# Kernel tuning notes

Measured on AMD Instinct MI355X. Metric: run time of the kernel, lower is better.

Reference implementation:

```python
import jax, jax.numpy as jnp
import numpy as np
import math

H_HEADS = 4
SQRT_2_PI = math.sqrt(2.0 / math.pi)


def _gelu_tanh(x):
    return 0.5 * x * (1.0 + jnp.tanh(SQRT_2_PI * (x + 0.044715 * x ** 3)))


def _ln(x, g, b, eps=1e-5):
    mu = jnp.mean(x, axis=-1, keepdims=True)
    var = jnp.var(x, axis=-1, keepdims=True)
    return g * (x - mu) * jax.lax.rsqrt(var + eps) + b


def _forward(support_emb_mat, query_t, support_t, cls_embed, t_freq, t_phase,
             Wq, bq, Wk, bk, Wv, bv, Wo, bo, ln1_g, ln1_b, time_w,
             W1, b1, W2, b2, ln2_g, ln2_b, Wc, bc, bn_g, bn_b):
    B, F, MD = support_emb_mat.shape
    Q = query_t.shape[1]
    S = F + 1
    H = H_HEADS
    D = MD * H
    dph = D // H
    L = Wq.shape[0]
    BQ = B * Q

    # [CLS] + support sequence, feature-tiled to model_dim*num_heads
    cls = jnp.broadcast_to(cls_embed, (B, 1, MD))
    seq = jnp.concatenate([cls, support_emb_mat], axis=1)          # [B,S,MD]
    x = jnp.tile(seq, (1, 1, H))                                    # [B,S,D]
    x = jnp.broadcast_to(x[:, None], (B, Q, S, D)).reshape(BQ, S, D)

    # time sequence: [query_t_q, support_t...] per (b,q)
    sup = jnp.broadcast_to(support_t[:, None, :], (B, Q, F))
    t_seq = jnp.concatenate([query_t[..., None], sup], axis=-1).reshape(BQ, S)
    t_diff = t_seq[:, :, None] - t_seq[:, None, :]                  # [BQ,S,S]
    # time encoder: cos(t*freq + phase) -> [BQ,S,S,TD]
    t_emb = jnp.cos(t_diff[..., None] * t_freq + t_phase)

    # scale as in source: (dim_per_head // num_heads) ** -0.5
    scale = (dph // H) ** (-0.5)

    for l in range(L):
        bias = t_emb @ time_w[l]                                    # [BQ,S,S]
        add = jnp.tile(bias, (H, 1, 1))                             # [BQ*H,S,S]
        res = x
        # raw row-major reshape to (BQ*H, S, dph) exactly as torch .view
        q = (x @ Wq[l] + bq[l]).reshape(BQ * H, S, dph)
        k = (x @ Wk[l] + bk[l]).reshape(BQ * H, S, dph)
        v = (x @ Wv[l] + bv[l]).reshape(BQ * H, S, dph)
        attn = jax.nn.softmax(jnp.einsum('bsd,btd->bst', q, k) * scale + add, axis=-1)
        ctx = jnp.einsum('bst,btd->bsd', attn, v).reshape(BQ, S, D)
        out = _ln(res + ctx @ Wo[l] + bo[l], ln1_g[l], ln1_b[l])
        ffn = _gelu_tanh(out @ W1[l] + b1[l]) @ W2[l] + b2[l]
        x = _ln(out + ffn, ln2_g[l], ln2_b[l])

    # compress: Linear -> BatchNorm1d over seq channels (train mode) -> LeakyReLU
    h = x @ Wc + bc                                                 # [BQ,S,MD]
    mu = jnp.mean(h, axis=(0, 2), keepdims=True)
    var = jnp.var(h, axis=(0, 2), keepdims=True)
    h = bn_g[None, :, None] * (h - mu) * jax.lax.rsqrt(var + 1e-5) + bn_b[None, :, None]
    h = jnp.where(h >= 0, h, 0.01 * h)                              # LeakyReLU
    return h[:, 0, :].reshape(B, Q, MD)


def setup_inputs() -> dict:
    key = jax.random.key(0)
    ks = jax.random.split(key, 24)
    B, Q, F, MD = 128, 32, 7, 128
    H, L, FFN, TD = 4, 6, 2048, 32
    S = F + 1
    D = MD * H

    def nrm(k, shape, s=0.02):
        return jax.random.normal(k, shape, jnp.float32) * s

    inp = {
        'support_emb_mat': jax.random.normal(ks[0], (B, F, MD), jnp.float32),
        'query_t': jax.random.uniform(ks[1], (B, Q), jnp.float32) * 100.0,
        'support_t': jax.random.uniform(ks[2], (B, F), jnp.float32) * 100.0,
        'cls_embed': jax.random.uniform(ks[3], (1, MD), jnp.float32),
        't_freq': nrm(ks[4], (TD,), 1.0),
        't_phase': nrm(ks[5], (TD,), 1.0),
        'Wq': nrm(ks[6], (L, D, D)), 'bq': jnp.zeros((L, D)),
        'Wk': nrm(ks[7], (L, D, D)), 'bk': jnp.zeros((L, D)),
        'Wv': nrm(ks[8], (L, D, D)), 'bv': jnp.zeros((L, D)),
        'Wo': nrm(ks[9], (L, D, D)), 'bo': jnp.zeros((L, D)),
        'ln1_g': jnp.ones((L, D)), 'ln1_b': jnp.zeros((L, D)),
        'time_w': jnp.ones((L, TD)) * 0.001,
        'W1': nrm(ks[10], (L, D, FFN)), 'b1': jnp.zeros((L, FFN)),
        'W2': nrm(ks[11], (L, FFN, D)), 'b2': jnp.zeros((L, D)),
        'ln2_g': jnp.ones((L, D)), 'ln2_b': jnp.zeros((L, D)),
        'Wc': nrm(ks[12], (D, MD)), 'bc': jnp.zeros((MD,)),
        'bn_g': jnp.ones((S,)), 'bn_b': jnp.zeros((S,)),
    }
    return inp


def reference(support_emb_mat, query_t, support_t, cls_embed, t_freq, t_phase,
              Wq, bq, Wk, bk, Wv, bv, Wo, bo, ln1_g, ln1_b, time_w,
              W1, b1, W2, b2, ln2_g, ln2_b, Wc, bc, bn_g, bn_b):
    return _forward(support_emb_mat, query_t, support_t, cls_embed, t_freq, t_phase,
                    Wq, bq, Wk, bk, Wv, bv, Wo, bo, ln1_g, ln1_b, time_w,
                    W1, b1, W2, b2, ln2_g, ln2_b, Wc, bc, bn_g, bn_b)
```

## Files before the change

### kernel.cpp

```cpp
#include <hip/hip_runtime.h>
#include <hip/hip_bf16.h>

typedef _Float16 f16;
typedef __attribute__((ext_vector_type(8))) _Float16 f16x8;
typedef __attribute__((ext_vector_type(4))) _Float16 f16x4;
typedef __attribute__((ext_vector_type(4))) float f32x4;

#define DEVI __device__ __forceinline__

DEVI float ldf(const void* p, size_t i, int isf32) {
    if (isf32) return ((const float*)p)[i];
    unsigned int u = ((const unsigned short*)p)[i];
    union { unsigned int b; float f; } c; c.b = u << 16;
    return c.f;
}

DEVI void gld_lds16(const f16* g, f16* l) {
    __builtin_amdgcn_global_load_lds(
        (__attribute__((address_space(1))) void*)(g),
        (__attribute__((address_space(3))) void*)(l), 16, 0, 0);
}

__global__ void detect_dtype(const void* qt, int* flag) {
    if (threadIdx.x == 0 && blockIdx.x == 0) {
        const unsigned int* w = (const unsigned int*)qt;
        int cnt = 0;
        for (int i = 0; i < 64; ++i) {
            unsigned int lo = w[i] & 0xFFFFu;
            union { unsigned int b; float f; } c; c.b = lo << 16;
            if (c.f >= 1e-4f && c.f <= 100.5f) ++cnt;
        }
        *flag = (cnt >= 32) ? 0 : 1;
    }
}

__global__ __launch_bounds__(256)
void cvt_in(const void* __restrict__ src, float* __restrict__ dst, int n,
            const int* __restrict__ flag) {
    const int f32 = *flag;
    int i = blockIdx.x * 256 + threadIdx.x;
    if (i < n) dst[i] = ldf(src, i, f32);
}

__global__ __launch_bounds__(256)
void fill_out(float* out, float v) {
    out[blockIdx.x * 256 + threadIdx.x] = v;
}

template<int EPI>
__global__ __launch_bounds__(512, 2)
void gemm256(const f16* __restrict__ Ag, const f16* __restrict__ BTg,
             const float* __restrict__ biasg, void* __restrict__ outg,
             int NZ, int gridN, int N, int K, int lda,
             long zsB, long zsBias, long zsC)
{
    const int tid = threadIdx.x;
    const int w = tid >> 6, lane = tid & 63;
    const int wm = w >> 2, wn = w & 3;
    const int r16 = lane & 15, q4 = lane >> 4;

    const int cpx = gridDim.x >> 3;
    const int id  = (blockIdx.x & 7) * cpx + (blockIdx.x >> 3);

    const int nz   = id % NZ;
    const int mloc = id / NZ;
    const int z    = nz / gridN;
    const int nt   = nz - z * gridN;
    const int tm = mloc * 256, tn = nt * 256;

    const f16*   BT   = BTg + (size_t)z * zsB;
    const float* bias = biasg + (size_t)z * zsBias;
    const size_t zoffC = (size_t)z * zsC;

    __shared__ __align__(16) f16 smA[2][2][16][64][8];
    __shared__ __align__(16) f16 smB[2][2][16][64][8];

    const f16* gA[4]; const f16* gB[4];
#pragma unroll
    for (int t = 0; t < 4; ++t) {
        const int c = 4 * w + t, kk = c >> 4, rc = c & 15;
        gA[t] = Ag + (size_t)(tm + rc * 16 + r16) * lda + kk * 32 + q4 * 8;
        gB[t] = BT + (size_t)(tn + rc * 16 + r16) * K  + kk * 32 + q4 * 8;
    }
    f16* const smAbase = &smA[0][0][0][0][0];
    f16* const smBbase = &smB[0][0][0][0][0];
    const int coff = (4 * w) * 512;

    auto issue = [&](int kt, int buf) {
        const size_t o = (size_t)kt * 64;
        const int bo = buf * 16384 + coff;
#pragma unroll
        for (int t = 0; t < 4; ++t) {
            gld_lds16(gA[t] + o, smAbase + bo + t * 512);
            gld_lds16(gB[t] + o, smBbase + bo + t * 512);
        }
    };

    f32x4 acc[8][4];
#pragma unroll
    for (int i = 0; i < 8; ++i)
#pragma unroll
        for (int j = 0; j < 4; ++j) acc[i][j] = (f32x4)0.0f;

    const int iters = K >> 6;
    issue(0, 0);
    __builtin_amdgcn_s_waitcnt(0x0F70);
    __builtin_amdgcn_s_barrier();
    __asm__ __volatile__("" ::: "memory");

    for (int kt = 0; kt < iters; ++kt) {
        const int cur = kt & 1;
        const bool more = (kt + 1 < iters);
        if (more) issue(kt + 1, cur ^ 1);
#pragma unroll
        for (int kk = 0; kk < 2; ++kk) {
            f16x8 af[8], bf[4];
#pragma unroll
            for (int i = 0; i < 8; ++i)
                af[i] = *(const f16x8*)&smA[cur][kk][wm * 8 + i][lane][0];
#pragma unroll
            for (int j = 0; j < 4; ++j)
                bf[j] = *(const f16x8*)&smB[cur][kk][wn * 4 + j][lane][0];
#pragma unroll
            for (int i = 0; i < 8; ++i)
#pragma unroll
                for (int j = 0; j < 4; ++j)
                    acc[i][j] = __builtin_amdgcn_mfma_f32_16x16x32_f16(
                        bf[j], af[i], acc[i][j], 0, 0, 0);
        }
        if (more) {
            __builtin_amdgcn_s_waitcnt(0x0F70);
            __builtin_amdgcn_s_barrier();
            __asm__ __volatile__("" ::: "memory");
        }
    }

    const int rowBase = tm + wm * 128;
    const int colBase = tn + wn * 64;
#pragma unroll
    for (int i = 0; i < 8; ++i) {
        const int row = rowBase + i * 16 + r16;
        const size_t rowoff = (size_t)row * N;
#pragma unroll
        for (int j = 0; j < 4; ++j) {
            const int n0 = colBase + j * 16 + q4 * 4;
            const f32x4 bv4 = *(const f32x4*)&bias[n0];
            f16x4 o;
#pragma unroll
            for (int r = 0; r < 4; ++r) {
                float v = acc[i][j][r] + bv4[r];
                if constexpr (EPI == 2) {
                    float v2 = v * v;
                    float t  = v * (1.0f + 0.044715f * v2);
                    float e  = __expf(1.5957691216057308f * t);
                    float rc = __builtin_amdgcn_rcpf(e + 1.0f);
                    v = v - v * rc;
                }
                o[r] = (f16)v;
            }
            *(f16x4*)((f16*)outg + zoffC + rowoff + n0) = o;
        }
    }
}

template<int EPI>
__global__ __launch_bounds__(256, 4)
void gemm_bt(const f16* __restrict__ Ag, const f16* __restrict__ BTg,
             const float* __restrict__ biasg, const f16* __restrict__ resg,
             void* __restrict__ outg,
             int NT, int NTZ, int MCHUNK, int MT, int N, int K, int lda,
             long zsB, long zsBias, long zsC)
{
    const int tid  = threadIdx.x;
    const int w    = tid >> 6, lane = tid & 63;
    const int wm   = w >> 1,   wn   = w & 1;

    const int id    = blockIdx.x;
    const int pc    = MCHUNK * NTZ;
    const int chunk = id / pc;
    const int rem   = id - chunk * pc;
    const int mloc  = rem % MCHUNK;
    const int ynz   = rem / MCHUNK;
    const int z     = ynz / NT;
    const int tmB   = (chunk * MCHUNK + mloc) * (128 * MT);
    const int tn    = (ynz - z * NT) * 128;

    const f16*   BT   = BTg + (size_t)z * zsB;
    const float* bias = biasg + (size_t)z * zsBias;
    const size_t zoffC = (size_t)z * zsC;

    __shared__ __align__(16) f16 smA[2][8][64][8];
    __shared__ __align__(16) f16 smB[2][8][64][8];

    const int r16 = lane & 15, q4 = lane >> 4;
    const int iters = K >> 5;

    const f16* gA0 = Ag + (size_t)(tmB + (2 * w) * 16 + r16) * lda + q4 * 8;
    const f16* gA1 = gA0 + (size_t)16 * lda;
    const f16* gB0 = BT + (size_t)(tn + (2 * w) * 16 + r16) * K + q4 * 8;
    const f16* gB1 = gB0 + (size_t)16 * K;

    auto issue = [&](int msN, int ktN, int buf) {
        const size_t aoff = (size_t)msN * 128 * lda + (size_t)ktN * 32;
        const size_t boff = (size_t)ktN * 32;
        gld_lds16(gA0 + aoff, &smA[buf][2 * w][0][0]);
        gld_lds16(gA1 + aoff, &smA[buf][2 * w + 1][0][0]);
        gld_lds16(gB0 + boff, &smB[buf][2 * w][0][0]);
        gld_lds16(gB1 + boff, &smB[buf][2 * w + 1][0][0]);
    };

    issue(0, 0, 0);
    int stage = 0;

    for (int ms = 0; ms < MT; ++ms) {
        const int tm = tmB + ms * 128;

        f32x4 acc[4][4];
#pragma unroll
        for (int i = 0; i < 4; ++i)
#pragma unroll
            for (int j = 0; j < 4; ++j) acc[i][j] = (f32x4)0.0f;

        for (int kt = 0; kt < iters; ++kt, ++stage) {
            const int cur = stage & 1;
            __builtin_amdgcn_s_barrier();
            int ktN = kt + 1, msN = ms;
            if (ktN == iters) { ktN = 0; ++msN; }
            if (msN < MT) {
                issue(msN, ktN, cur ^ 1);
                __builtin_amdgcn_s_waitcnt(0x0F74);
            } else {
                __builtin_amdgcn_s_waitcnt(0x0F70);
            }
            __builtin_amdgcn_s_barrier();
            __asm__ __volatile__("" ::: "memory");

            f16x8 af[4], bf[4];
#pragma unroll
            for (int i = 0; i < 4; ++i) {
                af[i] = *(const f16x8*)&smA[cur][wm * 4 + i][lane][0];
                bf[i] = *(const f16x8*)&smB[cur][wn * 4 + i][lane][0];
            }
#pragma unroll
            for (int i = 0; i < 4; ++i)
#pragma unroll
                for (int j = 0; j < 4; ++j)
                    acc[i][j] = __builtin_amdgcn_mfma_f32_16x16x32_f16(
                        bf[j], af[i], acc[i][j], 0, 0, 0);
        }

        const int rowBase = tm + wm * 64;
        const int colBase = tn + wn * 64;
#pragma unroll
        for (int i = 0; i < 4; ++i) {
            const int row = rowBase + i * 16 + r16;
            const size_t rowoff = (size_t)row * N;
#pragma unroll
            for (int j = 0; j < 4; ++j) {
                const int n0 = colBase + j * 16 + q4 * 4;
                const f32x4 bv4 = *(const f32x4*)&bias[n0];
                if constexpr (EPI == 3) {
                    f32x4 o;
#pragma unroll
                    for (int r = 0; r < 4; ++r) o[r] = acc[i][j][r] + bv4[r];
                    *(f32x4*)((float*)outg + rowoff + n0) = o;
                } else {
                    f16x4 o;
#pragma unroll
                    for (int r = 0; r < 4; ++r) {
                        float v = acc[i][j][r] + bv4[r];
                        if constexpr (EPI == 2) {
                            float v2 = v * v;
                            float t  = v * (1.0f + 0.044715f * v2);
                            float e  = __expf(1.5957691216057308f * t);
                            float rc = __builtin_amdgcn_rcpf(e + 1.0f);
                            v = v - v * rc;
                        }
                        o[r] = (f16)v;
                    }
                    *(f16x4*)((f16*)outg + zoffC + rowoff + n0) = o;
                }
            }
        }
    }
}

__global__ __launch_bounds__(512, 2)
void gemm_ln(const f16* __restrict__ Ag, const f16* __restrict__ BTg,
             const float* __restrict__ bias, const f16* __restrict__ resg,
             const float* __restrict__ lng, const float* __restrict__ lnb,
             f16* __restrict__ Yg, int K, int lda)
{
    const int tid = threadIdx.x;
    const int w = tid >> 6, lane = tid & 63;
    const int wm = w >> 2, wn = w & 3;
    const int r16 = lane & 15, q4 = lane >> 4;
    const int tm = blockIdx.x * 128;

    __shared__ __align__(16) f16 smA[2][8][64][8];
    __shared__ __align__(16) f16 smB[2][32][64][8];
    __shared__ __align__(16) float lnS[128][4];
    __shared__ __align__(16) float lnQ[128][4];

    f32x4 acc[4][8];
#pragma unroll
    for (int i = 0; i < 4; ++i)
#pragma unroll
        for (int j = 0; j < 8; ++j) acc[i][j] = (f32x4)0.0f;

    const f16* gA  = Ag  + (size_t)(tm + w * 16 + r16) * lda + q4 * 8;
    const f16* gB  = BTg + (size_t)(w * 64 + r16) * K + q4 * 8;
    const int iters = K >> 5;

    auto issue = [&](int kt, int buf) {
        const size_t o = (size_t)kt * 32;
        gld_lds16(gA + o, &smA[buf][w][0][0]);
#pragma unroll
        for (int t = 0; t < 4; ++t)
            gld_lds16(gB + (size_t)(t * 16) * K + o, &smB[buf][w * 4 + t][0][0]);
    };

    issue(0, 0);
    for (int kt = 0; kt < iters; ++kt) {
        const int cur = kt & 1;
        __builtin_amdgcn_s_barrier();
        if (kt + 1 < iters) {
            issue(kt + 1, cur ^ 1);
            __builtin_amdgcn_s_waitcnt(0x0F75);
        } else {
            __builtin_amdgcn_s_waitcnt(0x0F70);
        }
        __builtin_amdgcn_s_barrier();
        __asm__ __volatile__("" ::: "memory");

        f16x8 af[4], bf[8];
#pragma unroll
        for (int i = 0; i < 4; ++i)
            af[i] = *(const f16x8*)&smA[cur][wm * 4 + i][lane][0];
#pragma unroll
        for (int j = 0; j < 8; ++j)
            bf[j] = *(const f16x8*)&smB[cur][wn * 8 + j][lane][0];
#pragma unroll
        for (int i = 0; i < 4; ++i)
#pragma unroll
            for (int j = 0; j < 8; ++j)
                acc[i][j] = __builtin_amdgcn_mfma_f32_16x16x32_f16(
                    bf[j], af[i], acc[i][j], 0, 0, 0);
    }

    const int rowB = wm * 64;
    const int colB = wn * 128;

    float ps[4], pq[4];
#pragma unroll
    for (int i = 0; i < 4; ++i) {
        const int grow = tm + rowB + i * 16 + r16;
        const size_t roff = (size_t)grow * 512;
        float s = 0.f, sq = 0.f;
#pragma unroll
        for (int j = 0; j < 8; ++j) {
            const int n0 = colB + j * 16 + q4 * 4;
            const f32x4 biv = *(const f32x4*)&bias[n0];
            const f16x4 rv  = *(const f16x4*)&resg[roff + n0];
#pragma unroll
            for (int r = 0; r < 4; ++r) {
                float v = acc[i][j][r] + biv[r] + (float)rv[r];
                acc[i][j][r] = v;
                s += v; sq += v * v;
            }
        }
        s  += __shfl_xor(s, 16, 64);  s  += __shfl_xor(s, 32, 64);
        sq += __shfl_xor(sq, 16, 64); sq += __shfl_xor(sq, 32, 64);
        ps[i] = s; pq[i] = sq;
    }
    if (q4 == 0) {
#pragma unroll
        for (int i = 0; i < 4; ++i) {
            const int lr = rowB + i * 16 + r16;
            lnS[lr][wn] = ps[i];
            lnQ[lr][wn] = pq[i];
        }
    }
    __syncthreads();

#pragma unroll
    for (int i = 0; i < 4; ++i) {
        const int lr = rowB + i * 16 + r16;
        const f32x4 s4 = *(const f32x4*)&lnS[lr][0];
        const f32x4 q4v = *(const f32x4*)&lnQ[lr][0];
        const float s  = s4[0] + s4[1] + s4[2] + s4[3];
        const float sq = q4v[0] + q4v[1] + q4v[2] + q4v[3];
        const float mu = s * (1.0f / 512.0f);
        const float var = sq * (1.0f / 512.0f) - mu * mu;
        const float rs = rsqrtf(var + 1e-5f);
        const size_t rowoff = (size_t)(tm + lr) * 512;
#pragma unroll
        for (int j = 0; j < 8; ++j) {
            const int n0 = colB + j * 16 + q4 * 4;
            const f32x4 g4 = *(const f32x4*)&lng[n0];
            const f32x4 b4 = *(const f32x4*)&lnb[n0];
            f16x4 o;
#pragma unroll
            for (int r = 0; r < 4; ++r)
                o[r] = (f16)(g4[r] * (acc[i][j][r] - mu) * rs + b4[r]);
            *(f16x4*)&Yg[rowoff + n0] = o;
        }
    }
}

__global__ __launch_bounds__(256)
void attn_kernel(const f16* __restrict__ qg, const f16* __restrict__ kg,
                 const f16* __restrict__ vg, const float* __restrict__ biasL,
                 f16* __restrict__ cg, int small)
{
    const int w = threadIdx.x >> 6, lane = threadIdx.x & 63;
    const int j = blockIdx.x * 4 + w;
    __shared__ __align__(16) f16 sQ[4][8][136];
    __shared__ __align__(16) f16 sK[4][8][136];
    __shared__ __align__(16) f16 sV[4][8][136];
    __shared__ float sP[4][8][8];

    const size_t base  = (size_t)j * 1024;
    const size_t ibase = small ? ((size_t)(j >> 7) * 4096 + (size_t)(j & 3) * 1024)
                               : base;
#pragma unroll
    for (int t = 0; t < 2; ++t) {
        int flat = (t * 64 + lane) * 8;
        int r = flat >> 7, c = flat & 127;
        *(f16x8*)&sQ[w][r][c] = *(const f16x8*)(qg + ibase + flat);
        *(f16x8*)&sK[w][r][c] = *(const f16x8*)(kg + ibase + flat);
        *(f16x8*)&sV[w][r][c] = *(const f16x8*)(vg + ibase + flat);
    }
    __syncthreads();

    const int i = lane >> 3, jj = lane & 7;
    float d = 0.f;
#pragma unroll
    for (int c = 0; c < 16; ++c) {
        f16x8 qv = *(const f16x8*)&sQ[w][i][c * 8];
        f16x8 kv = *(const f16x8*)&sK[w][jj][c * 8];
#pragma unroll
        for (int e = 0; e < 8; ++e) d += (float)qv[e] * (float)kv[e];
    }
    float s = d * 0.17677669529663687f + biasL[(size_t)(j & 4095) * 64 + lane];
    float mx = s;
    mx = fmaxf(mx, __shfl_xor(mx, 1, 64));
    mx = fmaxf(mx, __shfl_xor(mx, 2, 64));
    mx = fmaxf(mx, __shfl_xor(mx, 4, 64));
    float p = __expf(s - mx);
    float sum = p;
    sum += __shfl_xor(sum, 1, 64);
    sum += __shfl_xor(sum, 2, 64);
    sum += __shfl_xor(sum, 4, 64);
    sP[w][i][jj] = p / sum;
    __syncthreads();

#pragma unroll
    for (int t2 = 0; t2 < 8; ++t2) {
        float ap[8];
#pragma unroll
        for (int e = 0; e < 8; ++e) ap[e] = sP[w][t2][e];
#pragma unroll
        for (int h = 0; h < 2; ++h) {
            int flat = (t2 * 2 + h) * 64 + lane;
            int dd = flat & 127;
            float o = 0.f;
#pragma unroll
            for (int e = 0; e < 8; ++e) o += ap[e] * (float)sV[w][e][dd];
            cg[base + flat] = (f16)o;
        }
    }
}

__global__ __launch_bounds__(256)
void build_x0(const void* __restrict__ sup, const void* __restrict__ cls,
              f16* __restrict__ xb, const int* __restrict__ flag)
{
    const int f32 = *flag;
    const size_t idx = ((size_t)blockIdx.x * 256 + threadIdx.x) * 4;
    const int row = (int)(idx >> 9), col0 = (int)(idx & 511);
    const int s = row & 7, b = row >> 8;
    f16x4 o;
#pragma unroll
    for (int e = 0; e < 4; ++e) {
        const int md = (col0 + e) & 127;
        float v = (s == 0) ? ldf(cls, md, f32)
                           : ldf(sup, ((size_t)b * 7 + (s - 1)) * 128 + md, f32);
        o[e] = (f16)v;
    }
    *(f16x4*)(xb + idx) = o;
}

__global__ __launch_bounds__(256)
void build_x0s(const void* __restrict__ sup, const void* __restrict__ cls,
               f16* __restrict__ xs, const int* __restrict__ flag)
{
    const int f32 = *flag;
    const size_t idx = ((size_t)blockIdx.x * 256 + threadIdx.x) * 4;
    const int row = (int)(idx >> 9), col0 = (int)(idx & 511);
    const int s = row & 7, b = row >> 3;
    f16x4 o;
#pragma unroll
    for (int e = 0; e < 4; ++e) {
        const int md = (col0 + e) & 127;
        float v = (s == 0) ? ldf(cls, md, f32)
                           : ldf(sup, ((size_t)b * 7 + (s - 1)) * 128 + md, f32);
        o[e] = (f16)v;
    }
    *(f16x4*)(xs + idx) = o;
}

__global__ __launch_bounds__(256)
void bias_kernel(const void* __restrict__ qt, const void* __restrict__ st,
                 const void* __restrict__ freq, const void* __restrict__ phase,
                 const void* __restrict__ tw, float* __restrict__ biasAll,
                 const int* __restrict__ flag)
{
    const int f32 = *flag;
    const int lane = threadIdx.x & 63;
    const int bq = blockIdx.x * 4 + (threadIdx.x >> 6);
    const int b = bq >> 5, qq = bq & 31;
    const int i = lane >> 3, jj = lane & 7;
    const float ti = (i  == 0) ? ldf(qt, b * 32 + qq, f32) : ldf(st, b * 7 + i  - 1, f32);
    const float tj = (jj == 0) ? ldf(qt, b * 32 + qq, f32) : ldf(st, b * 7 + jj - 1, f32);
    const float td = ti - tj;
    float a[6] = {0.f, 0.f, 0.f, 0.f, 0.f, 0.f};
    for (int t = 0; t < 32; ++t) {
        float c = __cosf(td * ldf(freq, t, f32) + ldf(phase, t, f32));
#pragma unroll
        for (int l = 0; l < 6; ++l) a[l] += c * ldf(tw, l * 32 + t, f32);
    }
#pragma unroll
    for (int l = 0; l < 6; ++l)
        biasAll[(size_t)l * (4096 * 64) + (size_t)bq * 64 + lane] = a[l];
}

__global__ __launch_bounds__(256)
void transpose_cvt(const void* __restrict__ W, f16* __restrict__ WT,
                   int K, int N, long zsW, long zsWT, const int* __restrict__ flag)
{
    const int f32 = *flag;
    const size_t zoff = (size_t)blockIdx.z * zsW;
    f16* WTz = WT + (size_t)blockIdx.z * zsWT;
    __shared__ float tile[64][65];
    const int tn = blockIdx.x * 64, tk = blockIdx.y * 64;
#pragma unroll
    for (int t = 0; t < 16; ++t) {
        int idx = t * 256 + threadIdx.x;
        int r = idx >> 6, c = idx & 63;
        tile[r][c] = ldf(W, zoff + (size_t)(tk + r) * N + tn + c, f32);
    }
    __syncthreads();
#pragma unroll
    for (int t = 0; t < 16; ++t) {
        int idx = t * 256 + threadIdx.x;
        int r = idx >> 6, c = idx & 63;
        WTz[(size_t)(tn + r) * K + tk + c] = (f16)tile[c][r];
    }
}

__global__ __launch_bounds__(256)
void gather_qkvb(const void* __restrict__ bq, const void* __restrict__ bk,
                 const void* __restrict__ bv, float* __restrict__ dst,
                 const int* __restrict__ flag)
{
    const int f32 = *flag;
    int i = blockIdx.x * 256 + threadIdx.x;
    if (i < 9216) {
        int z = i / 3072, rem = i % 3072;
        const void* src = (z == 0) ? bq : ((z == 1) ? bk : bv);
        dst[i] = ldf(src, rem, f32);
    }
}

__global__ __launch_bounds__(256)
void bn_reduce(const float* __restrict__ h0, float* __restrict__ stats)
{
    const int t = blockIdx.x * 256 + threadIdx.x;
    float s = 0.f, ss = 0.f;
#pragma unroll
    for (int k = 0; k < 8; ++k) {
        float v = h0[t + k * 65536];
        s += v; ss += v * v;
    }
#pragma unroll
    for (int m = 1; m <= 32; m <<= 1) {
        s  += __shfl_xor(s, m, 64);
        ss += __shfl_xor(ss, m, 64);
    }
    __shared__ float ls[8];
    const int w = threadIdx.x >> 6, lane = threadIdx.x & 63;
    if (lane == 0) { ls[w] = s; ls[4 + w] = ss; }
    __syncthreads();
    if (threadIdx.x == 0) {
        atomicAdd(&stats[0], ls[0] + ls[1] + ls[2] + ls[3]);
        atomicAdd(&stats[1], ls[4] + ls[5] + ls[6] + ls[7]);
    }
}

__global__ __launch_bounds__(256)
void bn_apply(const float* __restrict__ h0, const float* __restrict__ stats,
              const float* __restrict__ bnp, float* __restrict__ out)
{
    const int t = blockIdx.x * 256 + threadIdx.x;
    const float mu  = stats[0] * (1.0f / 524288.0f);
    const float var = stats[1] * (1.0f / 524288.0f) - mu * mu;
    const float rs  = rsqrtf(var + 1e-5f);
    float v = bnp[0] * (h0[t] - mu) * rs + bnp[8];
    v = (v >= 0.f) ? v : 0.01f * v;
    out[t] = v;
}

extern "C" void kernel_launch(void* const* d_in, const int* in_sizes, int n_in,
                              void* d_out, int out_size, void* d_ws, size_t ws_size,
                              hipStream_t stream)
{
    (void)in_sizes; (void)n_in; (void)out_size;
    const void* sup   = d_in[0];
    const void* qt    = d_in[1];
    const void* st    = d_in[2];
    const void* cls   = d_in[3];
    const void* freq  = d_in[4];
    const void* phase = d_in[5];
    const void* Wq = d_in[6];  const void* bqv = d_in[7];
    const void* Wk = d_in[8];  const void* bkv = d_in[9];
    const void* Wv = d_in[10]; const void* bvv = d_in[11];
    const void* Wo = d_in[12]; const void* bo  = d_in[13];
    const void* ln1g = d_in[14]; const void* ln1b = d_in[15];
    const void* tw = d_in[16];
    const void* W1 = d_in[17]; const void* b1 = d_in[18];
    const void* W2 = d_in[19]; const void* b2 = d_in[20];
    const void* ln2g = d_in[21]; const void* ln2b = d_in[22];
    const void* Wc = d_in[23]; const void* bc = d_in[24];
    const void* bng = d_in[25]; const void* bnb = d_in[26];

    const size_t NEEDED = 245658240;
    if (ws_size < NEEDED) {
        fill_out<<<2048, 256, 0, stream>>>((float*)d_out, 999.0f);
        return;
    }

    char* ws = (char*)d_ws;
    f16*   wt      = (f16*)(ws + 0);
    float* biasAll = (float*)(ws + 37879808);
    float* qkvb    = (float*)(ws + 44171264);
    float* prm     = (float*)(ws + 44208128);
    float* stats   = (float*)(ws + 44331584);
    int*   flag    = (int*)  (ws + 44331592);
    f16*   xb      = (f16*)(ws + 44331648);
    f16*   ob      = (f16*)(ws + 77886080);
    char*  region  = ws + 111440512;
    f16*   qb      = (f16*)(region);
    f16*   kb      = (f16*)(region + 33554432);
    f16*   vb      = (f16*)(region + 67108864);
    f16*   cb      = (f16*)(region + 100663296);
    f16*   qs      = (f16*)(region);
    f16*   xs      = (f16*)(region + 100663296);
    f16*   fbuf    = (f16*)(region);
    float* h0      = (float*)(region);

    detect_dtype<<<1, 64, 0, stream>>>(qt, flag);

    cvt_in<<<12, 256, 0, stream>>>(bo,   prm + 0,     3072,  flag);
    cvt_in<<<48, 256, 0, stream>>>(b1,   prm + 3072,  12288, flag);
    cvt_in<<<12, 256, 0, stream>>>(b2,   prm + 15360, 3072,  flag);
    cvt_in<<<1,  256, 0, stream>>>(bc,   prm + 18432, 128,   flag);
    cvt_in<<<12, 256, 0, stream>>>(ln1g, prm + 18560, 3072,  flag);
    cvt_in<<<12, 256, 0, stream>>>(ln1b, prm + 21632, 3072,  flag);
    cvt_in<<<12, 256, 0, stream>>>(ln2g, prm + 24704, 3072,  flag);
    cvt_in<<<12, 256, 0, stream>>>(ln2b, prm + 27776, 3072,  flag);
    cvt_in<<<1,  256, 0, stream>>>(bng,  prm + 30848, 8,     flag);
    cvt_in<<<1,  256, 0, stream>>>(bnb,  prm + 30856, 8,     flag);

    transpose_cvt<<<dim3(8, 8, 6),  256, 0, stream>>>(Wq, wt + 0,        512, 512,  262144, 262144, flag);
    transpose_cvt<<<dim3(8, 8, 6),  256, 0, stream>>>(Wk, wt + 1572864,  512, 512,  262144, 262144, flag);
    transpose_cvt<<<dim3(8, 8, 6),  256, 0, stream>>>(Wv, wt + 3145728,  512, 512,  262144, 262144, flag);
    transpose_cvt<<<dim3(8, 8, 6),  256, 0, stream>>>(Wo, wt + 4718592,  512, 512,  262144, 262144, flag);
    transpose_cvt<<<dim3(32, 8, 6), 256, 0, stream>>>(W1, wt + 6291456,  512, 2048, 1048576, 1048576, flag);
    transpose_cvt<<<dim3(8, 32, 6), 256, 0, stream>>>(W2, wt + 12582912, 2048, 512, 1048576, 1048576, flag);
    transpose_cvt<<<dim3(2, 8, 1),  256, 0, stream>>>(Wc, wt + 18874368, 512, 128,  0, 0, flag);
    gather_qkvb<<<36, 256, 0, stream>>>(bqv, bkv, bvv, qkvb, flag);
    build_x0<<<16384, 256, 0, stream>>>(sup, cls, xb, flag);
    build_x0s<<<512, 256, 0, stream>>>(sup, cls, xs, flag);
    bias_kernel<<<1024, 256, 0, stream>>>(qt, st, freq, phase, tw, biasAll, flag);
    hipMemsetAsync(stats, 0, 8, stream);

    for (int l = 0; l < 6; ++l) {
        if (l == 0) {
            gemm256<0><<<24, 512, 0, stream>>>(
                xs, wt, qkvb, qs,
                6, 2, 512, 512, 512, 1572864, 3072, 524288);
            attn_kernel<<<4096, 256, 0, stream>>>(
                qs, qs + 524288, qs + 1048576, biasAll, cb, 1);
        } else {
            gemm256<0><<<768, 512, 0, stream>>>(
                xb, wt + l * 262144, qkvb + l * 512, qb,
                6, 2, 512, 512, 512, 1572864, 3072, 16777216);
            attn_kernel<<<4096, 256, 0, stream>>>(
                qb, kb, vb, biasAll + (size_t)l * 262144, cb, 0);
        }
        gemm_ln<<<256, 512, 0, stream>>>(
            cb, wt + 4718592 + l * 262144, prm + 0 + l * 512, xb,
            prm + 18560 + l * 512, prm + 21632 + l * 512, ob, 512, 512);
        gemm256<2><<<1024, 512, 0, stream>>>(
            ob, wt + 6291456 + l * 1048576, prm + 3072 + l * 2048, fbuf,
            8, 8, 2048, 512, 512, 0, 0, 0);
        gemm_ln<<<256, 512, 0, stream>>>(
            fbuf, wt + 12582912 + l * 1048576, prm + 15360 + l * 512, ob,
            prm + 24704 + l * 512, prm + 27776 + l * 512, xb, 2048, 2048);
    }

    gemm_bt<3><<<32, 256, 0, stream>>>(
        xb, wt + 18874368, prm + 18432, nullptr, h0,
        1, 1, 32, 1, 128, 512, 4096 , 0, 0, 0);
    bn_reduce<<<256, 256, 0, stream>>>(h0, stats);
    bn_apply<<<2048, 256, 0, stream>>>(h0, stats, prm + 30848, (float*)d_out);
}
```

Baseline: 2.837 ms.

## Replace double-buffered K=64 GEMM loop with 4-stage K=32 LDS pipeline

Changes the GEMM mainloop from two LDS buffers holding 64-wide K tiles to four buffers holding 32-wide K tiles, keeping three tiles in flight. Partial vmcnt waits replace the full drain before each barrier, so global-to-LDS loads overlap MFMA work over more stages. The cost is a barrier every 32 K-elements instead of every 64, and fewer MFMAs per barrier. Total LDS size stays the same.

```diff
diff --git a/kernel.cpp b/kernel.cpp
--- a/kernel.cpp
+++ b/kernel.cpp
@@ -72,27 +72,24 @@
     const float* bias = biasg + (size_t)z * zsBias;
     const size_t zoffC = (size_t)z * zsC;
 
-    __shared__ __align__(16) f16 smA[2][2][16][64][8];
-    __shared__ __align__(16) f16 smB[2][2][16][64][8];
-
-    const f16* gA[4]; const f16* gB[4];
-#pragma unroll
-    for (int t = 0; t < 4; ++t) {
-        const int c = 4 * w + t, kk = c >> 4, rc = c & 15;
-        gA[t] = Ag + (size_t)(tm + rc * 16 + r16) * lda + kk * 32 + q4 * 8;
-        gB[t] = BT + (size_t)(tn + rc * 16 + r16) * K  + kk * 32 + q4 * 8;
-    }
-    f16* const smAbase = &smA[0][0][0][0][0];
-    f16* const smBbase = &smB[0][0][0][0][0];
-    const int coff = (4 * w) * 512;
-
-    auto issue = [&](int kt, int buf) {
-        const size_t o = (size_t)kt * 64;
-        const int bo = buf * 16384 + coff;
-#pragma unroll
-        for (int t = 0; t < 4; ++t) {
-            gld_lds16(gA[t] + o, smAbase + bo + t * 512);
-            gld_lds16(gB[t] + o, smBbase + bo + t * 512);
+    __shared__ __align__(16) f16 smA[4][16][64][8];
+    __shared__ __align__(16) f16 smB[4][16][64][8];
+
+    const f16* gA[2]; const f16* gB[2];
+#pragma unroll
+    for (int t = 0; t < 2; ++t) {
+        const int rc = 2 * w + t;
+        gA[t] = Ag + (size_t)(tm + rc * 16 + r16) * lda + q4 * 8;
+        gB[t] = BT + (size_t)(tn + rc * 16 + r16) * K  + q4 * 8;
+    }
+
+    auto issue = [&](int kt) {
+        const int buf = kt & 3;
+        const size_t o = (size_t)kt * 32;
+#pragma unroll
+        for (int t = 0; t < 2; ++t) {
+            gld_lds16(gA[t] + o, &smA[buf][2 * w + t][0][0]);
+            gld_lds16(gB[t] + o, &smB[buf][2 * w + t][0][0]);
         }
     };
 
@@ -102,37 +99,32 @@
 #pragma unroll
         for (int j = 0; j < 4; ++j) acc[i][j] = (f32x4)0.0f;
 
-    const int iters = K >> 6;
-    issue(0, 0);
-    __builtin_amdgcn_s_waitcnt(0x0F70);
-    __builtin_amdgcn_s_barrier();
-    __asm__ __volatile__("" ::: "memory");
+    const int iters = K >> 5;
+    issue(0); issue(1); issue(2);
 
     for (int kt = 0; kt < iters; ++kt) {
-        const int cur = kt & 1;
-        const bool more = (kt + 1 < iters);
-        if (more) issue(kt + 1, cur ^ 1);
-#pragma unroll
-        for (int kk = 0; kk < 2; ++kk) {
-            f16x8 af[8], bf[4];
-#pragma unroll
-            for (int i = 0; i < 8; ++i)
-                af[i] = *(const f16x8*)&smA[cur][kk][wm * 8 + i][lane][0];
+        if (kt + 2 < iters)      __builtin_amdgcn_s_waitcnt(0x0F78);
+        else if (kt + 1 < iters) __builtin_amdgcn_s_waitcnt(0x0F74);
+        else                     __builtin_amdgcn_s_waitcnt(0x0F70);
+        __asm__ __volatile__("" ::: "memory");
+        __builtin_amdgcn_s_barrier();
+        __asm__ __volatile__("" ::: "memory");
+        if (kt + 3 < iters) issue(kt + 3);
+
+        const int cur = kt & 3;
+        f16x8 af[8], bf[4];
+#pragma unroll
+        for (int i = 0; i < 8; ++i)
+            af[i] = *(const f16x8*)&smA[cur][wm * 8 + i][lane][0];
+#pragma unroll
+        for (int j = 0; j < 4; ++j)
+            bf[j] = *(const f16x8*)&smB[cur][wn * 4 + j][lane][0];
+#pragma unroll
+        for (int i = 0; i < 8; ++i)
 #pragma unroll
             for (int j = 0; j < 4; ++j)
-                bf[j] = *(const f16x8*)&smB[cur][kk][wn * 4 + j][lane][0];
-#pragma unroll
-            for (int i = 0; i < 8; ++i)
-#pragma unroll
-                for (int j = 0; j < 4; ++j)
-                    acc[i][j] = __builtin_amdgcn_mfma_f32_16x16x32_f16(
-                        bf[j], af[i], acc[i][j], 0, 0, 0);
-        }
-        if (more) {
-            __builtin_amdgcn_s_waitcnt(0x0F70);
-            __builtin_amdgcn_s_barrier();
-            __asm__ __volatile__("" ::: "memory");
-        }
+                acc[i][j] = __builtin_amdgcn_mfma_f32_16x16x32_f16(
+                    bf[j], af[i], acc[i][j], 0, 0, 0);
     }
 
     const int rowBase = tm + wm * 128;
```

Result: no change. 2.859 ms (+0.8%).

## Compute only CLS-row query path in final layer and simplify classifier GEMM

Applied to the files above, without the earlier changes.

In the last transformer layer, only the CLS token's output is consumed by the classifier, so Q, attention output, Wo, FFN and layer norms are computed just for the first row of each sequence. K and V are still computed for all rows. The attention kernel gains a mode that loads a single query row per head slice and writes fewer output rows. The classifier GEMM is replaced by a simpler single-tile kernel reading the compacted CLS rows. This relies on the strided row layout and the new residual stride parameter being correct.

```diff
diff --git a/kernel.cpp b/kernel.cpp
--- a/kernel.cpp
+++ b/kernel.cpp
@@ -165,25 +165,24 @@
 
 template<int EPI>
 __global__ __launch_bounds__(256, 4)
-void gemm_bt(const f16* __restrict__ Ag, const f16* __restrict__ BTg,
-             const float* __restrict__ biasg, const f16* __restrict__ resg,
-             void* __restrict__ outg,
-             int NT, int NTZ, int MCHUNK, int MT, int N, int K, int lda,
-             long zsB, long zsBias, long zsC)
+void gemm_bt2(const f16* __restrict__ Ag, const f16* __restrict__ BTg,
+              const float* __restrict__ biasg, void* __restrict__ outg,
+              int NZ, int gridN, int N, int K, int lda,
+              long zsB, long zsBias, long zsC)
 {
     const int tid  = threadIdx.x;
     const int w    = tid >> 6, lane = tid & 63;
     const int wm   = w >> 1,   wn   = w & 1;
-
-    const int id    = blockIdx.x;
-    const int pc    = MCHUNK * NTZ;
-    const int chunk = id / pc;
-    const int rem   = id - chunk * pc;
-    const int mloc  = rem % MCHUNK;
-    const int ynz   = rem / MCHUNK;
-    const int z     = ynz / NT;
-    const int tmB   = (chunk * MCHUNK + mloc) * (128 * MT);
-    const int tn    = (ynz - z * NT) * 128;
+    const int r16  = lane & 15, q4 = lane >> 4;
+
+    const int cpx = gridDim.x >> 3;
+    const int id  = (blockIdx.x & 7) * cpx + (blockIdx.x >> 3);
+
+    const int nz   = id % NZ;
+    const int mloc = id / NZ;
+    const int z    = nz / gridN;
+    const int nt   = nz - z * gridN;
+    const int tm   = mloc * 128, tn = nt * 128;
 
     const f16*   BT   = BTg + (size_t)z * zsB;
     const float* bias = biasg + (size_t)z * zsBias;
@@ -192,94 +191,84 @@
     __shared__ __align__(16) f16 smA[2][8][64][8];
     __shared__ __align__(16) f16 smB[2][8][64][8];
 
-    const int r16 = lane & 15, q4 = lane >> 4;
     const int iters = K >> 5;
 
-    const f16* gA0 = Ag + (size_t)(tmB + (2 * w) * 16 + r16) * lda + q4 * 8;
+    const f16* gA0 = Ag + (size_t)(tm + (2 * w) * 16 + r16) * lda + q4 * 8;
     const f16* gA1 = gA0 + (size_t)16 * lda;
     const f16* gB0 = BT + (size_t)(tn + (2 * w) * 16 + r16) * K + q4 * 8;
     const f16* gB1 = gB0 + (size_t)16 * K;
 
-    auto issue = [&](int msN, int ktN, int buf) {
-        const size_t aoff = (size_t)msN * 128 * lda + (size_t)ktN * 32;
-        const size_t boff = (size_t)ktN * 32;
-        gld_lds16(gA0 + aoff, &smA[buf][2 * w][0][0]);
-        gld_lds16(gA1 + aoff, &smA[buf][2 * w + 1][0][0]);
-        gld_lds16(gB0 + boff, &smB[buf][2 * w][0][0]);
-        gld_lds16(gB1 + boff, &smB[buf][2 * w + 1][0][0]);
+    auto issue = [&](int kt, int buf) {
+        const size_t o = (size_t)kt * 32;
+        gld_lds16(gA0 + o, &smA[buf][2 * w][0][0]);
+        gld_lds16(gA1 + o, &smA[buf][2 * w + 1][0][0]);
+        gld_lds16(gB0 + o, &smB[buf][2 * w][0][0]);
+        gld_lds16(gB1 + o, &smB[buf][2 * w + 1][0][0]);
     };
 
-    issue(0, 0, 0);
-    int stage = 0;
-
-    for (int ms = 0; ms < MT; ++ms) {
-        const int tm = tmB + ms * 128;
-
-        f32x4 acc[4][4];
+    f32x4 acc[4][4];
+#pragma unroll
+    for (int i = 0; i < 4; ++i)
+#pragma unroll
+        for (int j = 0; j < 4; ++j) acc[i][j] = (f32x4)0.0f;
+
+    issue(0, 0);
+    for (int kt = 0; kt < iters; ++kt) {
+        const int cur = kt & 1;
+        __builtin_amdgcn_s_barrier();
+        if (kt + 1 < iters) {
+            issue(kt + 1, cur ^ 1);
+            __builtin_amdgcn_s_waitcnt(0x0F74);
+        } else {
+            __builtin_amdgcn_s_waitcnt(0x0F70);
+        }
+        __builtin_amdgcn_s_barrier();
+        __asm__ __volatile__("" ::: "memory");
+
+        f16x8 af[4], bf[4];
+#pragma unroll
+        for (int i = 0; i < 4; ++i) {
+            af[i] = *(const f16x8*)&smA[cur][wm * 4 + i][lane][0];
+            bf[i] = *(const f16x8*)&smB[cur][wn * 4 + i][lane][0];
+        }
 #pragma unroll
         for (int i = 0; i < 4; ++i)
 #pragma unroll
-            for (int j = 0; j < 4; ++j) acc[i][j] = (f32x4)0.0f;
-
-        for (int kt = 0; kt < iters; ++kt, ++stage) {
-            const int cur = stage & 1;
-            __builtin_amdgcn_s_barrier();
-            int ktN = kt + 1, msN = ms;
-            if (ktN == iters) { ktN = 0; ++msN; }
-            if (msN < MT) {
-                issue(msN, ktN, cur ^ 1);
-                __builtin_amdgcn_s_waitcnt(0x0F74);
+            for (int j = 0; j < 4; ++j)
+                acc[i][j] = __builtin_amdgcn_mfma_f32_16x16x32_f16(
+                    bf[j], af[i], acc[i][j], 0, 0, 0);
+    }
+
+    const int rowBase = tm + wm * 64;
+    const int colBase = tn + wn * 64;
+#pragma unroll
+    for (int i = 0; i < 4; ++i) {
+        const int row = rowBase + i * 16 + r16;
+        const size_t rowoff = (size_t)row * N;
+#pragma unroll
+        for (int j = 0; j < 4; ++j) {
+            const int n0 = colBase + j * 16 + q4 * 4;
+            const f32x4 bv4 = *(const f32x4*)&bias[n0];
+            if constexpr (EPI == 3) {
+                f32x4 o;
+#pragma unroll
+                for (int r = 0; r < 4; ++r) o[r] = acc[i][j][r] + bv4[r];
+                *(f32x4*)((float*)outg + rowoff + n0) = o;
             } else {
-                __builtin_amdgcn_s_waitcnt(0x0F70);
-            }
-            __builtin_amdgcn_s_barrier();
-            __asm__ __volatile__("" ::: "memory");
-
-            f16x8 af[4], bf[4];
-#pragma unroll
-            for (int i = 0; i < 4; ++i) {
-                af[i] = *(const f16x8*)&smA[cur][wm * 4 + i][lane][0];
-                bf[i] = *(const f16x8*)&smB[cur][wn * 4 + i][lane][0];
-            }
-#pragma unroll
-            for (int i = 0; i < 4; ++i)
-#pragma unroll
-                for (int j = 0; j < 4; ++j)
-                    acc[i][j] = __builtin_amdgcn_mfma_f32_16x16x32_f16(
-                        bf[j], af[i], acc[i][j], 0, 0, 0);
-        }
-
-        const int rowBase = tm + wm * 64;
-        const int colBase = tn + wn * 64;
-#pragma unroll
-        for (int i = 0; i < 4; ++i) {
-            const int row = rowBase + i * 16 + r16;
-            const size_t rowoff = (size_t)row * N;
-#pragma unroll
-            for (int j = 0; j < 4; ++j) {
-                const int n0 = colBase + j * 16 + q4 * 4;
-                const f32x4 bv4 = *(const f32x4*)&bias[n0];
-                if constexpr (EPI == 3) {
-                    f32x4 o;
-#pragma unroll
-                    for (int r = 0; r < 4; ++r) o[r] = acc[i][j][r] + bv4[r];
-                    *(f32x4*)((float*)outg + rowoff + n0) = o;
-                } else {
-                    f16x4 o;
-#pragma unroll
-                    for (int r = 0; r < 4; ++r) {
-                        float v = acc[i][j][r] + bv4[r];
-                        if constexpr (EPI == 2) {
-                            float v2 = v * v;
-                            float t  = v * (1.0f + 0.044715f * v2);
-                            float e  = __expf(1.5957691216057308f * t);
-                            float rc = __builtin_amdgcn_rcpf(e + 1.0f);
-                            v = v - v * rc;
-                        }
-                        o[r] = (f16)v;
+                f16x4 o;
+#pragma unroll
+                for (int r = 0; r < 4; ++r) {
+                    float v = acc[i][j][r] + bv4[r];
+                    if constexpr (EPI == 2) {
+                        float v2 = v * v;
+                        float t  = v * (1.0f + 0.044715f * v2);
+                        float e  = __expf(1.5957691216057308f * t);
+                        float rc = __builtin_amdgcn_rcpf(e + 1.0f);
+                        v = v - v * rc;
                     }
-                    *(f16x4*)((f16*)outg + zoffC + rowoff + n0) = o;
+                    o[r] = (f16)v;
                 }
+                *(f16x4*)((f16*)outg + zoffC + rowoff + n0) = o;
             }
         }
     }
@@ -289,7 +278,7 @@
 void gemm_ln(const f16* __restrict__ Ag, const f16* __restrict__ BTg,
              const float* __restrict__ bias, const f16* __restrict__ resg,
              const float* __restrict__ lng, const float* __restrict__ lnb,
-             f16* __restrict__ Yg, int K, int lda)
+             f16* __restrict__ Yg, int K, int lda, int rstride)
 {
     const int tid = threadIdx.x;
     const int w = tid >> 6, lane = tid & 63;
@@ -355,7 +344,7 @@
 #pragma unroll
     for (int i = 0; i < 4; ++i) {
         const int grow = tm + rowB + i * 16 + r16;
-        const size_t roff = (size_t)grow * 512;
+        const size_t roff = (size_t)grow * rstride;
         float s = 0.f, sq = 0.f;
 #pragma unroll
         for (int j = 0; j < 8; ++j) {
@@ -411,7 +400,7 @@
 __global__ __launch_bounds__(256)
 void attn_kernel(const f16* __restrict__ qg, const f16* __restrict__ kg,
                  const f16* __restrict__ vg, const float* __restrict__ biasL,
-                 f16* __restrict__ cg, int small)
+                 f16* __restrict__ cg, int mode)
 {
     const int w = threadIdx.x >> 6, lane = threadIdx.x & 63;
     const int j = blockIdx.x * 4 + w;
@@ -420,16 +409,37 @@
     __shared__ __align__(16) f16 sV[4][8][136];
     __shared__ float sP[4][8][8];
 
-    const size_t base  = (size_t)j * 1024;
-    const size_t ibase = small ? ((size_t)(j >> 7) * 4096 + (size_t)(j & 3) * 1024)
-                               : base;
-#pragma unroll
-    for (int t = 0; t < 2; ++t) {
-        int flat = (t * 64 + lane) * 8;
-        int r = flat >> 7, c = flat & 127;
-        *(f16x8*)&sQ[w][r][c] = *(const f16x8*)(qg + ibase + flat);
-        *(f16x8*)&sK[w][r][c] = *(const f16x8*)(kg + ibase + flat);
-        *(f16x8*)&sV[w][r][c] = *(const f16x8*)(vg + ibase + flat);
+    size_t base, biasrow;
+    if (mode == 2) {
+        base = (size_t)j * 4096;
+        biasrow = (size_t)((j << 2) & 4095);
+        {
+            int flat = lane * 8;
+            *(f16x8*)&sQ[w][flat >> 7][flat & 127] =
+                *(const f16x8*)(qg + (size_t)j * 512 + flat);
+            int f2 = 512 + lane * 8;
+            *(f16x8*)&sQ[w][f2 >> 7][f2 & 127] = (f16x8)(f16)0.0f;
+        }
+#pragma unroll
+        for (int t = 0; t < 2; ++t) {
+            int flat = (t * 64 + lane) * 8;
+            int r = flat >> 7, c = flat & 127;
+            *(f16x8*)&sK[w][r][c] = *(const f16x8*)(kg + base + flat);
+            *(f16x8*)&sV[w][r][c] = *(const f16x8*)(vg + base + flat);
+        }
+    } else {
+        base = (size_t)j * 1024;
+        biasrow = (size_t)(j & 4095);
+        const size_t ibase = (mode == 1)
+            ? ((size_t)(j >> 7) * 4096 + (size_t)(j & 3) * 1024) : base;
+#pragma unroll
+        for (int t = 0; t < 2; ++t) {
+            int flat = (t * 64 + lane) * 8;
+            int r = flat >> 7, c = flat & 127;
+            *(f16x8*)&sQ[w][r][c] = *(const f16x8*)(qg + ibase + flat);
+            *(f16x8*)&sK[w][r][c] = *(const f16x8*)(kg + ibase + flat);
+            *(f16x8*)&sV[w][r][c] = *(const f16x8*)(vg + ibase + flat);
+        }
     }
     __syncthreads();
 
@@ -442,7 +452,7 @@
 #pragma unroll
         for (int e = 0; e < 8; ++e) d += (float)qv[e] * (float)kv[e];
     }
-    float s = d * 0.17677669529663687f + biasL[(size_t)(j & 4095) * 64 + lane];
+    float s = d * 0.17677669529663687f + biasL[biasrow * 64 + lane];
     float mx = s;
     mx = fmaxf(mx, __shfl_xor(mx, 1, 64));
     mx = fmaxf(mx, __shfl_xor(mx, 2, 64));
@@ -455,8 +465,8 @@
     sP[w][i][jj] = p / sum;
     __syncthreads();
 
-#pragma unroll
-    for (int t2 = 0; t2 < 8; ++t2) {
+    const int nrows = (mode == 2) ? 4 : 8;
+    for (int t2 = 0; t2 < nrows; ++t2) {
         float ap[8];
 #pragma unroll
         for (int e = 0; e < 8; ++e) ap[e] = sP[w][t2][e];
@@ -692,27 +702,51 @@
                 6, 2, 512, 512, 512, 1572864, 3072, 524288);
             attn_kernel<<<4096, 256, 0, stream>>>(
                 qs, qs + 524288, qs + 1048576, biasAll, cb, 1);
-        } else {
+        } else if (l < 5) {
             gemm256<0><<<768, 512, 0, stream>>>(
                 xb, wt + l * 262144, qkvb + l * 512, qb,
                 6, 2, 512, 512, 512, 1572864, 3072, 16777216);
             attn_kernel<<<4096, 256, 0, stream>>>(
                 qb, kb, vb, biasAll + (size_t)l * 262144, cb, 0);
-        }
-        gemm_ln<<<256, 512, 0, stream>>>(
-            cb, wt + 4718592 + l * 262144, prm + 0 + l * 512, xb,
-            prm + 18560 + l * 512, prm + 21632 + l * 512, ob, 512, 512);
-        gemm256<2><<<1024, 512, 0, stream>>>(
-            ob, wt + 6291456 + l * 1048576, prm + 3072 + l * 2048, fbuf,
-            8, 8, 2048, 512, 512, 0, 0, 0);
-        gemm_ln<<<256, 512, 0, stream>>>(
-            fbuf, wt + 12582912 + l * 1048576, prm + 15360 + l * 512, ob,
-            prm + 24704 + l * 512, prm + 27776 + l * 512, xb, 2048, 2048);
-    }
-
-    gemm_bt<3><<<32, 256, 0, stream>>>(
-        xb, wt + 18874368, prm + 18432, nullptr, h0,
-        1, 1, 32, 1, 128, 512, 4096 , 0, 0, 0);
+        } else {
+            gemm256<0><<<64, 512, 0, stream>>>(
+                xb, wt + l * 262144 + 1572864, qkvb + l * 512 + 3072, kb,
+                4, 2, 4096, 512, 4096, 1572864, 3072, 16777216);
+            gemm256<0><<<64, 512, 0, stream>>>(
+                xb + 512, wt + l * 262144 + 1572864, qkvb + l * 512 + 3072, kb + 512,
+                4, 2, 4096, 512, 4096, 1572864, 3072, 16777216);
+            gemm256<0><<<32, 512, 0, stream>>>(
+                xb, wt + l * 262144, qkvb + l * 512, qb,
+                2, 2, 512, 512, 4096, 0, 0, 0);
+            attn_kernel<<<1024, 256, 0, stream>>>(
+                qb, kb, vb, biasAll + (size_t)l * 262144, cb, 2);
+        }
+        if (l < 5) {
+            gemm_ln<<<256, 512, 0, stream>>>(
+                cb, wt + 4718592 + l * 262144, prm + 0 + l * 512, xb,
+                prm + 18560 + l * 512, prm + 21632 + l * 512, ob, 512, 512, 512);
+            gemm256<2><<<1024, 512, 0, stream>>>(
+                ob, wt + 6291456 + l * 1048576, prm + 3072 + l * 2048, fbuf,
+                8, 8, 2048, 512, 512, 0, 0, 0);
+            gemm_ln<<<256, 512, 0, stream>>>(
+                fbuf, wt + 12582912 + l * 1048576, prm + 15360 + l * 512, ob,
+                prm + 24704 + l * 512, prm + 27776 + l * 512, xb, 2048, 2048, 512);
+        } else {
+            gemm_ln<<<32, 512, 0, stream>>>(
+                cb, wt + 4718592 + l * 262144, prm + 0 + l * 512, xb,
+                prm + 18560 + l * 512, prm + 21632 + l * 512, ob, 512, 4096, 4096);
+            gemm256<2><<<128, 512, 0, stream>>>(
+                ob, wt + 6291456 + l * 1048576, prm + 3072 + l * 2048, fbuf,
+                8, 8, 2048, 512, 512, 0, 0, 0);
+            gemm_ln<<<32, 512, 0, stream>>>(
+                fbuf, wt + 12582912 + l * 1048576, prm + 15360 + l * 512, ob,
+                prm + 24704 + l * 512, prm + 27776 + l * 512, cb, 2048, 2048, 512);
+        }
+    }
+
+    gemm_bt2<3><<<32, 256, 0, stream>>>(
+        cb, wt + 18874368, prm + 18432, h0,
+        1, 1, 128, 512, 512, 0, 0, 0);
     bn_reduce<<<256, 256, 0, stream>>>(h0, stats);
     bn_apply<<<2048, 256, 0, stream>>>(h0, stats, prm + 30848, (float*)d_out);
 }
```

Measured after the change: 2.719 ms. 4.2% less time.
